# Performance work log

Hardware: AMD Instinct MI355X
Metric: run time of the kernel (lower is better)

The kernel has to match this reference:

```python
import jax, jax.numpy as jnp
import numpy as np

K = 7            # kernel size per spatial dim
HALF = K // 2    # 3
WIN = K * K      # 49


def _rel_dist():
    # matches torch: meshgrid('ij') of arange(k)-k//2, euclidean dist, flattened row-major
    c = np.arange(K, dtype=np.float32) - HALF
    gi, gj = np.meshgrid(c, c, indexing='ij')
    return jnp.asarray(np.sqrt(gi ** 2 + gj ** 2).reshape(-1))


def _unfold2d(t):
    B, H, W, C = t.shape
    p = jnp.pad(t, ((0, 0), (HALF, HALF), (HALF, HALF), (0, 0)))
    wins = [p[:, i:i + H, j:j + W, :] for i in range(K) for j in range(K)]
    return jnp.stack(wins, axis=3)


def setup_inputs() -> dict:
    key = jax.random.key(0)
    k1, k2, k3, k4, k5 = jax.random.split(key, 5)
    B, H, W, C = 4, 64, 64, 128
    x = jax.random.normal(k1, (B, H, W, C), dtype=jnp.float32)
    W_qkv = jax.random.normal(k2, (C, 3 * C), dtype=jnp.float32) * (C ** -0.5)
    # width_proj is zero-initialized in the module; use small random values to exercise the soft mask
    W_width = jax.random.normal(k3, (C, 1), dtype=jnp.float32) * 0.02
    b_width = jax.random.normal(k4, (1,), dtype=jnp.float32) * 0.02
    W_out = jax.random.normal(k5, (C, C), dtype=jnp.float32) * (C ** -0.5)
    return {"x": x, "W_qkv": W_qkv, "W_width": W_width, "b_width": b_width, "W_out": W_out}


def reference(x, W_qkv, W_width, b_width, W_out):
    B, H, W, C = x.shape
    L = H * W
    scale = C ** -0.5
    rel_dist = _rel_dist()
    max_dist = rel_dist.max()

    qkv = x @ W_qkv                              # (B,H,W,3C)
    q, k, v = jnp.split(qkv, 3, axis=-1)
    width = jax.nn.sigmoid(x @ W_width + b_width) * max_dist + 0.5  # (B,H,W,1)

    k_win = _unfold2d(k).reshape(B, L, WIN, C)
    v_win = _unfold2d(v).reshape(B, L, WIN, C)
    q_flat = q.reshape(B, L, C)
    width_flat = width.reshape(B, L, 1)

    scores = jnp.einsum('blc,blwc->blw', q_flat, k_win) * scale
    soft_mask = jax.nn.sigmoid((width_flat - rel_dist) * 5.0)
    scores = scores - (1.0 - soft_mask) * 10000.0
    attn = jax.nn.softmax(scores, axis=-1)
    out = jnp.einsum('blw,blwc->blc', attn, v_win).reshape(B, H, W, C)
    return (out + v) @ W_out
```

## Files before the change

### kernel.cpp

```cpp
#include <hip/hip_runtime.h>

#define C 128
#define NPIX 16384
#define THREE_C 384

typedef unsigned short u16;
typedef unsigned int u32;
typedef short bf16x8 __attribute__((ext_vector_type(8)));
typedef float f32x4 __attribute__((ext_vector_type(4)));

__device__ __forceinline__ float bf2f(u16 h) { return __uint_as_float(((u32)h) << 16); }
__device__ __forceinline__ u16 f2bf(float f) {
    u32 b = __float_as_uint(f);
    b += 0x7FFF + ((b >> 16) & 1);
    return (u16)(b >> 16);
}
__device__ __forceinline__ u32 pack2(float a, float b) {
    return (u32)f2bf(a) | ((u32)f2bf(b) << 16);
}

#define GST 136

__global__ __launch_bounds__(512) void qkv_kernel(const float* __restrict__ x,
                                                  const float* __restrict__ Wqkv,
                                                  const float* __restrict__ Wwidth,
                                                  const float* __restrict__ bwidth,
                                                  u16* __restrict__ qb,
                                                  u16* __restrict__ kb,
                                                  u16* __restrict__ vb,
                                                  float* __restrict__ width_g) {
    __shared__ u16 xs[128 * GST];
    __shared__ u16 wt[128 * GST];
    const int task = ((int)(blockIdx.x & 7)) * 48 + ((int)blockIdx.x >> 3);
    const int rb = task / 3;
    const int nb = task % 3;
    const int p0 = rb * 128;
    const int tid = threadIdx.x;
    const int wv = tid >> 6;
    const int l = tid & 63;
    const int l15 = l & 15;
    const int l4 = l >> 4;

    for (int f = tid; f < 4096; f += 512) {
        const int kq = f & 31, r = f >> 5;
        const float4 xv = *(const float4*)(x + (size_t)(p0 + r) * C + kq * 4);
        uint2 pk;
        pk.x = pack2(xv.x, xv.y);
        pk.y = pack2(xv.z, xv.w);
        *(uint2*)&xs[r * GST + kq * 4] = pk;
    }
    for (int f = tid; f < 4096; f += 512) {
        const int c = f & 127, kq = f >> 7;
        const float w0 = Wqkv[(size_t)(kq * 4 + 0) * THREE_C + nb * 128 + c];
        const float w1 = Wqkv[(size_t)(kq * 4 + 1) * THREE_C + nb * 128 + c];
        const float w2 = Wqkv[(size_t)(kq * 4 + 2) * THREE_C + nb * 128 + c];
        const float w3 = Wqkv[(size_t)(kq * 4 + 3) * THREE_C + nb * 128 + c];
        uint2 pk;
        pk.x = pack2(w0, w1);
        pk.y = pack2(w2, w3);
        *(uint2*)&wt[c * GST + kq * 4] = pk;
    }
    __syncthreads();

    if (nb == 0 && tid < 128) {
        float wacc = 0.f;
#pragma unroll
        for (int kk = 0; kk < C; ++kk) wacc += bf2f(xs[tid * GST + kk]) * Wwidth[kk];
        const float z = wacc + bwidth[0];
        width_g[p0 + tid] = (1.f / (1.f + __expf(-z))) * 4.242640687f + 0.5f;
    }

    const int strip = wv * 16;
    bf16x8 af[4];
#pragma unroll
    for (int kf = 0; kf < 4; ++kf)
        af[kf] = *(const bf16x8*)&xs[(strip + l15) * GST + kf * 32 + l4 * 8];

    f32x4 acc[8];
#pragma unroll
    for (int nf = 0; nf < 8; ++nf) acc[nf] = (f32x4){0.f, 0.f, 0.f, 0.f};
#pragma unroll
    for (int nf = 0; nf < 8; ++nf) {
#pragma unroll
        for (int kf = 0; kf < 4; ++kf) {
            const bf16x8 bf = *(const bf16x8*)&wt[(nf * 16 + l15) * GST + kf * 32 + l4 * 8];
            acc[nf] = __builtin_amdgcn_mfma_f32_16x16x32_bf16(af[kf], bf, acc[nf], 0, 0, 0);
        }
    }

    u16* dst = (nb == 0) ? qb : (nb == 1) ? kb : vb;
#pragma unroll
    for (int nf = 0; nf < 8; ++nf) {
        const int col = nf * 16 + l15;
#pragma unroll
        for (int r = 0; r < 4; ++r) {
            const int row = strip + l4 * 4 + r;
            dst[(size_t)(p0 + row) * C + col] = f2bf(acc[nf][r]);
        }
    }
}

#define HSTRIDE 136
#define TSTRIDE 232

__global__ __launch_bounds__(1024) void attn_kernel(const u16* __restrict__ qb,
                                                    const u16* __restrict__ kb,
                                                    const u16* __restrict__ vb,
                                                    const float* __restrict__ width_g,
                                                    const float* __restrict__ Wout,
                                                    float* __restrict__ out) {
    __shared__ u16 Kl[208 * HSTRIDE];
    __shared__ u16 Vt[128 * TSTRIDE];
    __shared__ u16 Pl[64 * TSTRIDE];
    __shared__ float rmax[4][64];
    __shared__ float rsum[4][64];
    __shared__ float wdl[64];

    const int tid = threadIdx.x;
    const int wv = tid >> 6;
    const int l = tid & 63;
    const int l15 = l & 15;
    const int l4 = l >> 4;

    const int W = ((int)blockIdx.x & 7) * 32 + ((int)blockIdx.x >> 3);
    const int b = W >> 6;
    const int t = W & 63;
    const int i0 = (t >> 3) * 8;
    const int j0 = (t & 7) * 8;
    const int pbase = b * 4096;

    if (tid < 64)
        wdl[tid] = width_g[pbase + (i0 + (tid >> 3)) * 64 + j0 + (tid & 7)];

    for (int f = tid; f < 3328; f += 1024) {
        const int c = f & 15, h = f >> 4;
        uint4 val = make_uint4(0, 0, 0, 0);
        if (h < 196) {
            const int hi = (h * 2341) >> 15;
            const int hj = h - hi * 14;
            const int ii = i0 - 3 + hi, jj = j0 - 3 + hj;
            if (((unsigned)ii < 64u) && ((unsigned)jj < 64u))
                val = *(const uint4*)(kb + (size_t)(pbase + ii * 64 + jj) * C + c * 8);
        }
        *(uint4*)&Kl[h * HSTRIDE + c * 8] = val;
    }
    for (int f = tid; f < 1792; f += 1024) {
        const int c8 = f & 15, h2 = f >> 4;
        const int h = h2 * 2;
        union { uint4 u4; u16 us[8]; } va, vz;
        va.u4 = make_uint4(0, 0, 0, 0);
        vz.u4 = make_uint4(0, 0, 0, 0);
        if (h < 196) {
            const int hi = (h * 2341) >> 15;
            const int hj = h - hi * 14;
            const int ii = i0 - 3 + hi, jj = j0 - 3 + hj;
            if (((unsigned)ii < 64u) && ((unsigned)jj < 64u))
                va.u4 = *(const uint4*)(vb + (size_t)(pbase + ii * 64 + jj) * C + c8 * 8);
        }
        if (h + 1 < 196) {
            const int hi = ((h + 1) * 2341) >> 15;
            const int hj = h + 1 - hi * 14;
            const int ii = i0 - 3 + hi, jj = j0 - 3 + hj;
            if (((unsigned)ii < 64u) && ((unsigned)jj < 64u))
                vz.u4 = *(const uint4*)(vb + (size_t)(pbase + ii * 64 + jj) * C + c8 * 8);
        }
#pragma unroll
        for (int s = 0; s < 8; ++s)
            *(u32*)&Vt[(c8 * 8 + s) * TSTRIDE + h] = (u32)va.us[s] | ((u32)vz.us[s] << 16);
    }

    const int strip = wv >> 2;
    const int g = wv & 3;
    bf16x8 qf[4];
    {
        const int qr = strip * 16 + l15;
        const int p = pbase + (i0 + (qr >> 3)) * 64 + j0 + (qr & 7);
#pragma unroll
        for (int kf = 0; kf < 4; ++kf)
            qf[kf] = *(const bf16x8*)(qb + (size_t)p * C + kf * 32 + l4 * 8);
    }
    __syncthreads();

    f32x4 sv[4];
#pragma unroll
    for (int tt = 0; tt < 4; ++tt) {
        const int nf = g + 4 * tt;
        f32x4 acc = {0.f, 0.f, 0.f, 0.f};
        if (nf < 13) {
            const u16* kr = Kl + (nf * 16 + l15) * HSTRIDE + l4 * 8;
#pragma unroll
            for (int kf = 0; kf < 4; ++kf)
                acc = __builtin_amdgcn_mfma_f32_16x16x32_bf16(
                    qf[kf], *(const bf16x8*)(kr + kf * 32), acc, 0, 0, 0);
        }
        sv[tt] = acc;
    }

    const int qrb = strip * 16 + l4 * 4;
    float wdr[4], mxr[4];
#pragma unroll
    for (int r = 0; r < 4; ++r) { wdr[r] = wdl[qrb + r]; mxr[r] = -3.0e38f; }
#pragma unroll
    for (int tt = 0; tt < 4; ++tt) {
        const int nf = g + 4 * tt;
        if (nf < 13) {
            const int n = nf * 16 + l15;
            const int hi = (n * 2341) >> 15;
            const int hj = n - hi * 14;
#pragma unroll
            for (int r = 0; r < 4; ++r) {
                const int qr = qrb + r;
                const int di = hi - 3 - (qr >> 3);
                const int dj = hj - 3 - (qr & 7);
                const bool valid = ((unsigned)(di + 3) <= 6u) && ((unsigned)(dj + 3) <= 6u);
                float s = -3.0e38f;
                if (valid) {
                    const float rd = sqrtf((float)(di * di + dj * dj));
                    const float sm = 1.f / (1.f + __expf(-5.f * (wdr[r] - rd)));
                    s = sv[tt][r] * 0.08838834765f - (1.f - sm) * 10000.f;
                }
                sv[tt][r] = s;
                mxr[r] = fmaxf(mxr[r], s);
            }
        } else {
#pragma unroll
            for (int r = 0; r < 4; ++r) sv[tt][r] = -3.0e38f;
        }
    }
#pragma unroll
    for (int r = 0; r < 4; ++r) {
        float m = mxr[r];
        m = fmaxf(m, __shfl_xor(m, 1));
        m = fmaxf(m, __shfl_xor(m, 2));
        m = fmaxf(m, __shfl_xor(m, 4));
        m = fmaxf(m, __shfl_xor(m, 8));
        mxr[r] = m;
    }
    float smr[4] = {0.f, 0.f, 0.f, 0.f};
#pragma unroll
    for (int tt = 0; tt < 4; ++tt) {
#pragma unroll
        for (int r = 0; r < 4; ++r) {
            const float e = __expf(sv[tt][r] - mxr[r]);
            sv[tt][r] = e;
            smr[r] += e;
        }
    }
#pragma unroll
    for (int r = 0; r < 4; ++r) {
        float s = smr[r];
        s += __shfl_xor(s, 1);
        s += __shfl_xor(s, 2);
        s += __shfl_xor(s, 4);
        s += __shfl_xor(s, 8);
        smr[r] = s;
    }
    if (l15 == 0) {
#pragma unroll
        for (int r = 0; r < 4; ++r) {
            rmax[g][qrb + r] = mxr[r];
            rsum[g][qrb + r] = smr[r];
        }
    }
    __syncthreads();

    u16* wtl = Kl;
    for (int f = tid; f < 4096; f += 1024) {
        const int c = f & 127, kq = f >> 7;
        const float w0 = Wout[(size_t)(kq * 4 + 0) * C + c];
        const float w1 = Wout[(size_t)(kq * 4 + 1) * C + c];
        const float w2 = Wout[(size_t)(kq * 4 + 2) * C + c];
        const float w3 = Wout[(size_t)(kq * 4 + 3) * C + c];
        uint2 pk;
        pk.x = pack2(w0, w1);
        pk.y = pack2(w2, w3);
        *(uint2*)&wtl[c * GST + kq * 4] = pk;
    }

    float fac[4];
#pragma unroll
    for (int r = 0; r < 4; ++r) {
        const int qr = qrb + r;
        const float m0 = rmax[0][qr], m1 = rmax[1][qr], m2 = rmax[2][qr], m3 = rmax[3][qr];
        const float mf = fmaxf(fmaxf(m0, m1), fmaxf(m2, m3));
        const float tot = rsum[0][qr] * __expf(m0 - mf) + rsum[1][qr] * __expf(m1 - mf)
                        + rsum[2][qr] * __expf(m2 - mf) + rsum[3][qr] * __expf(m3 - mf);
        fac[r] = __expf(mxr[r] - mf) / tot;
    }
#pragma unroll
    for (int tt = 0; tt < 4; ++tt) {
        const int nf = g + 4 * tt;
        if (nf < 13) {
            const int n = nf * 16 + l15;
#pragma unroll
            for (int r = 0; r < 4; ++r)
                Pl[(qrb + r) * TSTRIDE + n] = f2bf(sv[tt][r] * fac[r]);
        } else if (nf == 13) {
            const int n = 208 + l15;
#pragma unroll
            for (int r = 0; r < 4; ++r)
                Pl[(qrb + r) * TSTRIDE + n] = 0;
        }
    }
    __syncthreads();

    f32x4 oacc[2];
    oacc[0] = (f32x4){0.f, 0.f, 0.f, 0.f};
    oacc[1] = (f32x4){0.f, 0.f, 0.f, 0.f};
#pragma unroll
    for (int kf = 0; kf < 7; ++kf) {
        const bf16x8 pa = *(const bf16x8*)(Pl + (strip * 16 + l15) * TSTRIDE + kf * 32 + l4 * 8);
#pragma unroll
        for (int nf2 = 0; nf2 < 2; ++nf2) {
            const bf16x8 vf = *(const bf16x8*)(Vt + (g * 32 + nf2 * 16 + l15) * TSTRIDE + kf * 32 + l4 * 8);
            oacc[nf2] = __builtin_amdgcn_mfma_f32_16x16x32_bf16(pa, vf, oacc[nf2], 0, 0, 0);
        }
    }
    __syncthreads();

    u16* ylds = Pl;
#pragma unroll
    for (int nf2 = 0; nf2 < 2; ++nf2) {
        const int cch = g * 32 + nf2 * 16 + l15;
#pragma unroll
        for (int r = 0; r < 4; ++r) {
            const int qr = qrb + r;
            const int h = 45 + (qr >> 3) * 14 + (qr & 7);
            const float vv = bf2f(Vt[cch * TSTRIDE + h]);
            ylds[qr * GST + cch] = f2bf(oacc[nf2][r] + vv);
        }
    }
    __syncthreads();

    bf16x8 yf[4];
#pragma unroll
    for (int kf = 0; kf < 4; ++kf)
        yf[kf] = *(const bf16x8*)&ylds[(strip * 16 + l15) * GST + kf * 32 + l4 * 8];

    f32x4 oc[2];
    oc[0] = (f32x4){0.f, 0.f, 0.f, 0.f};
    oc[1] = (f32x4){0.f, 0.f, 0.f, 0.f};
#pragma unroll
    for (int u = 0; u < 2; ++u) {
        const int nf = g + 4 * u;
#pragma unroll
        for (int kf = 0; kf < 4; ++kf) {
            const bf16x8 bf = *(const bf16x8*)&wtl[(nf * 16 + l15) * GST + kf * 32 + l4 * 8];
            oc[u] = __builtin_amdgcn_mfma_f32_16x16x32_bf16(yf[kf], bf, oc[u], 0, 0, 0);
        }
    }
#pragma unroll
    for (int u = 0; u < 2; ++u) {
        const int col = (g + 4 * u) * 16 + l15;
#pragma unroll
        for (int r = 0; r < 4; ++r) {
            const int qr = qrb + r;
            const int p = pbase + (i0 + (qr >> 3)) * 64 + j0 + (qr & 7);
            out[(size_t)p * C + col] = oc[u][r];
        }
    }
}

extern "C" void kernel_launch(void* const* d_in, const int* in_sizes, int n_in,
                              void* d_out, int out_size, void* d_ws, size_t ws_size,
                              hipStream_t stream) {
    const float* x      = (const float*)d_in[0];
    const float* Wqkv   = (const float*)d_in[1];
    const float* Wwidth = (const float*)d_in[2];
    const float* bwidth = (const float*)d_in[3];
    const float* Wout   = (const float*)d_in[4];
    float* out = (float*)d_out;

    u16* qb = (u16*)d_ws;
    u16* kb = qb + (size_t)NPIX * C;
    u16* vb = kb + (size_t)NPIX * C;
    float* width = (float*)(vb + (size_t)NPIX * C);

    qkv_kernel<<<384, 512, 0, stream>>>(x, Wqkv, Wwidth, bwidth, qb, kb, vb, width);
    attn_kernel<<<256, 1024, 0, stream>>>(qb, kb, vb, width, Wout, out);
}
```

Baseline: 30.70 us.

## Prefetch loads into registers, swizzle V transpose, drop x LDS staging

The QKV kernel now loads x fragments straight into registers instead of staging them through LDS, and computes the width projection in fp32 from global memory using four threads per row and shuffles. The attention kernel issues all K/V gather loads into registers before the Q loads and LDS stores, prefetches Wout before the softmax phase, and applies an XOR swizzle to the transposed V layout to reduce LDS bank conflicts. It also moves the y staging buffer into spare Kl space so one barrier can be dropped. The aim is to hide global latency and cut LDS conflicts, at the cost of higher register pressure with 1024-thread blocks.

```diff
diff --git a/kernel.cpp b/kernel.cpp
--- a/kernel.cpp
+++ b/kernel.cpp
@@ -29,7 +29,6 @@
                                                   u16* __restrict__ kb,
                                                   u16* __restrict__ vb,
                                                   float* __restrict__ width_g) {
-    __shared__ u16 xs[128 * GST];
     __shared__ u16 wt[128 * GST];
     const int task = ((int)(blockIdx.x & 7)) * 48 + ((int)blockIdx.x >> 3);
     const int rb = task / 3;
@@ -41,40 +40,58 @@
     const int l15 = l & 15;
     const int l4 = l >> 4;
 
-    for (int f = tid; f < 4096; f += 512) {
-        const int kq = f & 31, r = f >> 5;
-        const float4 xv = *(const float4*)(x + (size_t)(p0 + r) * C + kq * 4);
+    float wr[8][4];
+#pragma unroll
+    for (int t = 0; t < 8; ++t) {
+        const int f = tid + t * 512;
+        const int c = f & 127, kq = f >> 7;
+#pragma unroll
+        for (int s = 0; s < 4; ++s)
+            wr[t][s] = Wqkv[(size_t)(kq * 4 + s) * THREE_C + nb * 128 + c];
+    }
+    const int prow = p0 + wv * 16 + l15;
+    float4 xa[4][2];
+#pragma unroll
+    for (int kf = 0; kf < 4; ++kf) {
+        xa[kf][0] = *(const float4*)(x + (size_t)prow * C + kf * 32 + l4 * 8);
+        xa[kf][1] = *(const float4*)(x + (size_t)prow * C + kf * 32 + l4 * 8 + 4);
+    }
+#pragma unroll
+    for (int t = 0; t < 8; ++t) {
+        const int f = tid + t * 512;
+        const int c = f & 127, kq = f >> 7;
         uint2 pk;
-        pk.x = pack2(xv.x, xv.y);
-        pk.y = pack2(xv.z, xv.w);
-        *(uint2*)&xs[r * GST + kq * 4] = pk;
-    }
-    for (int f = tid; f < 4096; f += 512) {
-        const int c = f & 127, kq = f >> 7;
-        const float w0 = Wqkv[(size_t)(kq * 4 + 0) * THREE_C + nb * 128 + c];
-        const float w1 = Wqkv[(size_t)(kq * 4 + 1) * THREE_C + nb * 128 + c];
-        const float w2 = Wqkv[(size_t)(kq * 4 + 2) * THREE_C + nb * 128 + c];
-        const float w3 = Wqkv[(size_t)(kq * 4 + 3) * THREE_C + nb * 128 + c];
-        uint2 pk;
-        pk.x = pack2(w0, w1);
-        pk.y = pack2(w2, w3);
+        pk.x = pack2(wr[t][0], wr[t][1]);
+        pk.y = pack2(wr[t][2], wr[t][3]);
         *(uint2*)&wt[c * GST + kq * 4] = pk;
     }
+    bf16x8 af[4];
+#pragma unroll
+    for (int kf = 0; kf < 4; ++kf) {
+        union { u32 u[4]; bf16x8 v; } pk;
+        pk.u[0] = pack2(xa[kf][0].x, xa[kf][0].y);
+        pk.u[1] = pack2(xa[kf][0].z, xa[kf][0].w);
+        pk.u[2] = pack2(xa[kf][1].x, xa[kf][1].y);
+        pk.u[3] = pack2(xa[kf][1].z, xa[kf][1].w);
+        af[kf] = pk.v;
+    }
+    if (nb == 0) {
+        const int r = tid >> 2, qtr = tid & 3;
+        float wacc = 0.f;
+#pragma unroll
+        for (int q4 = 0; q4 < 8; ++q4) {
+            const float4 xv = *(const float4*)(x + (size_t)(p0 + r) * C + qtr * 32 + q4 * 4);
+            wacc += xv.x * Wwidth[qtr * 32 + q4 * 4 + 0] + xv.y * Wwidth[qtr * 32 + q4 * 4 + 1]
+                  + xv.z * Wwidth[qtr * 32 + q4 * 4 + 2] + xv.w * Wwidth[qtr * 32 + q4 * 4 + 3];
+        }
+        wacc += __shfl_xor(wacc, 1);
+        wacc += __shfl_xor(wacc, 2);
+        if (qtr == 0) {
+            const float z = wacc + bwidth[0];
+            width_g[p0 + r] = (1.f / (1.f + __expf(-z))) * 4.242640687f + 0.5f;
+        }
+    }
     __syncthreads();
-
-    if (nb == 0 && tid < 128) {
-        float wacc = 0.f;
-#pragma unroll
-        for (int kk = 0; kk < C; ++kk) wacc += bf2f(xs[tid * GST + kk]) * Wwidth[kk];
-        const float z = wacc + bwidth[0];
-        width_g[p0 + tid] = (1.f / (1.f + __expf(-z))) * 4.242640687f + 0.5f;
-    }
-
-    const int strip = wv * 16;
-    bf16x8 af[4];
-#pragma unroll
-    for (int kf = 0; kf < 4; ++kf)
-        af[kf] = *(const bf16x8*)&xs[(strip + l15) * GST + kf * 32 + l4 * 8];
 
     f32x4 acc[8];
 #pragma unroll
@@ -89,6 +106,7 @@
     }
 
     u16* dst = (nb == 0) ? qb : (nb == 1) ? kb : vb;
+    const int strip = wv * 16;
 #pragma unroll
     for (int nf = 0; nf < 8; ++nf) {
         const int col = nf * 16 + l15;
@@ -102,6 +120,7 @@
 
 #define HSTRIDE 136
 #define TSTRIDE 232
+#define VSWZ(ch, h) ((h) ^ ((((ch) >> 3) & 3) << 3))
 
 __global__ __launch_bounds__(1024) void attn_kernel(const u16* __restrict__ qb,
                                                     const u16* __restrict__ kb,
@@ -132,43 +151,55 @@
     if (tid < 64)
         wdl[tid] = width_g[pbase + (i0 + (tid >> 3)) * 64 + j0 + (tid & 7)];
 
-    for (int f = tid; f < 3328; f += 1024) {
-        const int c = f & 15, h = f >> 4;
-        uint4 val = make_uint4(0, 0, 0, 0);
-        if (h < 196) {
+    const uint4 z4 = make_uint4(0, 0, 0, 0);
+    uint4 kreg[4];
+    int kh[4], kc[4];
+    bool kok[4];
+#pragma unroll
+    for (int rr = 0; rr < 4; ++rr) {
+        const int f = tid + rr * 1024;
+        kok[rr] = (f < 3136);
+        kreg[rr] = z4;
+        kh[rr] = 0; kc[rr] = 0;
+        if (kok[rr]) {
+            const int c = f & 15, h = f >> 4;
+            kh[rr] = h; kc[rr] = c;
             const int hi = (h * 2341) >> 15;
             const int hj = h - hi * 14;
             const int ii = i0 - 3 + hi, jj = j0 - 3 + hj;
             if (((unsigned)ii < 64u) && ((unsigned)jj < 64u))
-                val = *(const uint4*)(kb + (size_t)(pbase + ii * 64 + jj) * C + c * 8);
-        }
-        *(uint4*)&Kl[h * HSTRIDE + c * 8] = val;
-    }
-    for (int f = tid; f < 1792; f += 1024) {
-        const int c8 = f & 15, h2 = f >> 4;
-        const int h = h2 * 2;
-        union { uint4 u4; u16 us[8]; } va, vz;
-        va.u4 = make_uint4(0, 0, 0, 0);
-        vz.u4 = make_uint4(0, 0, 0, 0);
-        if (h < 196) {
-            const int hi = (h * 2341) >> 15;
-            const int hj = h - hi * 14;
-            const int ii = i0 - 3 + hi, jj = j0 - 3 + hj;
-            if (((unsigned)ii < 64u) && ((unsigned)jj < 64u))
-                va.u4 = *(const uint4*)(vb + (size_t)(pbase + ii * 64 + jj) * C + c8 * 8);
-        }
-        if (h + 1 < 196) {
-            const int hi = ((h + 1) * 2341) >> 15;
-            const int hj = h + 1 - hi * 14;
-            const int ii = i0 - 3 + hi, jj = j0 - 3 + hj;
-            if (((unsigned)ii < 64u) && ((unsigned)jj < 64u))
-                vz.u4 = *(const uint4*)(vb + (size_t)(pbase + ii * 64 + jj) * C + c8 * 8);
-        }
-#pragma unroll
-        for (int s = 0; s < 8; ++s)
-            *(u32*)&Vt[(c8 * 8 + s) * TSTRIDE + h] = (u32)va.us[s] | ((u32)vz.us[s] << 16);
-    }
-
+                kreg[rr] = *(const uint4*)(kb + (size_t)(pbase + ii * 64 + jj) * C + c * 8);
+        }
+    }
+    uint4 va[2], vz[2];
+    int vc8[2], vh[2];
+    bool vok[2];
+#pragma unroll
+    for (int rr = 0; rr < 2; ++rr) {
+        const int f = tid + rr * 1024;
+        vok[rr] = (f < 1792);
+        va[rr] = z4; vz[rr] = z4;
+        vc8[rr] = 0; vh[rr] = 0;
+        if (vok[rr]) {
+            const int c8 = f & 15, h = (f >> 4) * 2;
+            vc8[rr] = c8; vh[rr] = h;
+            {
+                const int hi = (h * 2341) >> 15;
+                const int hj = h - hi * 14;
+                const int ii = i0 - 3 + hi, jj = j0 - 3 + hj;
+                if ((h < 196) && ((unsigned)ii < 64u) && ((unsigned)jj < 64u))
+                    va[rr] = *(const uint4*)(vb + (size_t)(pbase + ii * 64 + jj) * C + c8 * 8);
+            }
+            {
+                const int h1 = h + 1;
+                const int hi = (h1 * 2341) >> 15;
+                const int hj = h1 - hi * 14;
+                const int ii = i0 - 3 + hi, jj = j0 - 3 + hj;
+                if ((h1 < 196) && ((unsigned)ii < 64u) && ((unsigned)jj < 64u))
+                    vz[rr] = *(const uint4*)(vb + (size_t)(pbase + ii * 64 + jj) * C + c8 * 8);
+            }
+        }
+    }
     const int strip = wv >> 2;
     const int g = wv & 3;
     bf16x8 qf[4];
@@ -179,6 +210,23 @@
         for (int kf = 0; kf < 4; ++kf)
             qf[kf] = *(const bf16x8*)(qb + (size_t)p * C + kf * 32 + l4 * 8);
     }
+#pragma unroll
+    for (int rr = 0; rr < 4; ++rr)
+        if (kok[rr]) *(uint4*)&Kl[kh[rr] * HSTRIDE + kc[rr] * 8] = kreg[rr];
+#pragma unroll
+    for (int rr = 0; rr < 2; ++rr) {
+        if (vok[rr]) {
+            union { uint4 u4; u16 us[8]; } ua, uz;
+            ua.u4 = va[rr]; uz.u4 = vz[rr];
+            const int c8 = vc8[rr], h = vh[rr];
+#pragma unroll
+            for (int s = 0; s < 8; ++s) {
+                const int ch = c8 * 8 + s;
+                *(u32*)&Vt[ch * TSTRIDE + VSWZ(ch, h)] =
+                    (u32)ua.us[s] | ((u32)uz.us[s] << 16);
+            }
+        }
+    }
     __syncthreads();
 
     f32x4 sv[4];
@@ -194,6 +242,16 @@
                     qf[kf], *(const bf16x8*)(kr + kf * 32), acc, 0, 0, 0);
         }
         sv[tt] = acc;
+    }
+
+    float wor[4][4];
+#pragma unroll
+    for (int tq = 0; tq < 4; ++tq) {
+        const int f = tid + tq * 1024;
+        const int c = f & 127, kq = f >> 7;
+#pragma unroll
+        for (int s = 0; s < 4; ++s)
+            wor[tq][s] = Wout[(size_t)(kq * 4 + s) * C + c];
     }
 
     const int qrb = strip * 16 + l4 * 4;
@@ -265,15 +323,13 @@
     __syncthreads();
 
     u16* wtl = Kl;
-    for (int f = tid; f < 4096; f += 1024) {
+#pragma unroll
+    for (int tq = 0; tq < 4; ++tq) {
+        const int f = tid + tq * 1024;
         const int c = f & 127, kq = f >> 7;
-        const float w0 = Wout[(size_t)(kq * 4 + 0) * C + c];
-        const float w1 = Wout[(size_t)(kq * 4 + 1) * C + c];
-        const float w2 = Wout[(size_t)(kq * 4 + 2) * C + c];
-        const float w3 = Wout[(size_t)(kq * 4 + 3) * C + c];
         uint2 pk;
-        pk.x = pack2(w0, w1);
-        pk.y = pack2(w2, w3);
+        pk.x = pack2(wor[tq][0], wor[tq][1]);
+        pk.y = pack2(wor[tq][2], wor[tq][3]);
         *(uint2*)&wtl[c * GST + kq * 4] = pk;
     }
 
@@ -312,13 +368,13 @@
         const bf16x8 pa = *(const bf16x8*)(Pl + (strip * 16 + l15) * TSTRIDE + kf * 32 + l4 * 8);
 #pragma unroll
         for (int nf2 = 0; nf2 < 2; ++nf2) {
-            const bf16x8 vf = *(const bf16x8*)(Vt + (g * 32 + nf2 * 16 + l15) * TSTRIDE + kf * 32 + l4 * 8);
+            const int ch = g * 32 + nf2 * 16 + l15;
+            const bf16x8 vf = *(const bf16x8*)(Vt + ch * TSTRIDE + VSWZ(ch, kf * 32 + l4 * 8));
             oacc[nf2] = __builtin_amdgcn_mfma_f32_16x16x32_bf16(pa, vf, oacc[nf2], 0, 0, 0);
         }
     }
-    __syncthreads();
-
-    u16* ylds = Pl;
+
+    u16* ylds = Kl + 128 * GST;
 #pragma unroll
     for (int nf2 = 0; nf2 < 2; ++nf2) {
         const int cch = g * 32 + nf2 * 16 + l15;
@@ -326,7 +382,7 @@
         for (int r = 0; r < 4; ++r) {
             const int qr = qrb + r;
             const int h = 45 + (qr >> 3) * 14 + (qr & 7);
-            const float vv = bf2f(Vt[cch * TSTRIDE + h]);
+            const float vv = bf2f(Vt[cch * TSTRIDE + VSWZ(cch, h)]);
             ylds[qr * GST + cch] = f2bf(oacc[nf2][r] + vv);
         }
     }
```

Measured after the change: 34.62 us. 1.13x slower.
